# Kernel optimization log

Hardware: AMD Instinct MI355X
Metric: run time of the kernel (lower is better)

## Reference

```python
import jax, jax.numpy as jnp
import numpy as np

D_MODEL = 1024
N_HEADS = 16
DEPTH = D_MODEL // N_HEADS
P_FEAT = 64
NEG_BIG = -1.0e9


def setup_inputs() -> dict:
    key = jax.random.key(0)
    ks = jax.random.split(key, 12)
    B, S = 4, 2048
    s = 1.0 / np.sqrt(D_MODEL)
    return {
        "q": jax.random.normal(ks[0], (B, S, D_MODEL), jnp.float32),
        "k": jax.random.normal(ks[1], (B, S, D_MODEL), jnp.float32),
        "v": jax.random.normal(ks[2], (B, S, D_MODEL), jnp.float32),
        "protocol_features": jax.random.normal(ks[3], (B, P_FEAT), jnp.float32),
        "mask": jax.random.randint(ks[4], (B, 1, 1, S), 0, 2).astype(jnp.float32),
        "wq": jax.random.normal(ks[5], (D_MODEL, D_MODEL), jnp.float32) * s,
        "bq": jnp.zeros((D_MODEL,), jnp.float32),
        "wk": jax.random.normal(ks[6], (D_MODEL, D_MODEL), jnp.float32) * s,
        "bk": jnp.zeros((D_MODEL,), jnp.float32),
        "wv": jax.random.normal(ks[7], (D_MODEL, D_MODEL), jnp.float32) * s,
        "bv": jnp.zeros((D_MODEL,), jnp.float32),
        "wg": jax.random.normal(ks[8], (P_FEAT, N_HEADS), jnp.float32) * (1.0 / np.sqrt(P_FEAT)),
        "bg": jnp.zeros((N_HEADS,), jnp.float32),
    }


def _split_heads(x, B):
    # [B,S,d_model] -> [B,H,S,depth]
    return x.reshape(B, -1, N_HEADS, DEPTH).transpose(0, 2, 1, 3)


def reference(q, k, v, protocol_features, mask, wq, bq, wk, bk, wv, bv, wg, bg):
    B = q.shape[0]
    qh = _split_heads(q @ wq + bq, B)
    kh = _split_heads(k @ wk + bk, B)
    vh = _split_heads(v @ wv + bv, B)
    # scaled QK^T: [B,H,S,S]
    logits = jnp.einsum("bhqd,bhkd->bhqk", qh, kh) / jnp.sqrt(jnp.float32(DEPTH))
    # per-head protocol gate (sigmoid), broadcast over q/k positions
    validity = jax.nn.sigmoid(protocol_features @ wg + bg)  # [B,H]
    logits = logits * validity[:, :, None, None]
    logits = logits + mask * NEG_BIG
    attn = jax.nn.softmax(logits, axis=-1)
    out = jnp.einsum("bhqk,bhkd->bhqd", attn, vh)
    concat = out.transpose(0, 2, 1, 3).reshape(B, -1, D_MODEL)
    return concat, attn
```

## Files before the change

### kernel.cpp

```cpp
#include <hip/hip_runtime.h>

#define S_LEN 2048
#define NB 4
#define NH 16
#define BHN 64
#define DM 1024
#define DEP 64
#define MROWS 8192

typedef __attribute__((ext_vector_type(8))) short short8;
typedef __attribute__((ext_vector_type(4))) short s16x4;
typedef __attribute__((ext_vector_type(4))) float f32x4;

#define MFMA_BF16(a, b, c) __builtin_amdgcn_mfma_f32_16x16x32_bf16((a), (b), (c), 0, 0, 0)

__device__ __forceinline__ void mfma16(const s16x4& a, const s16x4& b, f32x4& c) {
  asm("v_mfma_f32_16x16x16_bf16 %0, %1, %2, %0" : "+v"(c) : "v"(a), "v"(b));
}

typedef __attribute__((address_space(1))) const void* as1cv;
typedef __attribute__((address_space(3))) void* as3v;

__device__ __forceinline__ void gld16(const void* g, void* l) {
  __builtin_amdgcn_global_load_lds((as1cv)g, (as3v)l, 16, 0, 0);
}

__device__ __forceinline__ unsigned short f2bf(float f) {
  unsigned u = __float_as_uint(f);
  u += 0x7fffu + ((u >> 16) & 1u);
  return (unsigned short)(u >> 16);
}

__device__ __forceinline__ unsigned cvtpk(float a, float b) {
  unsigned r;
  asm("v_cvt_pk_bf16_f32 %0, %1, %2" : "=v"(r) : "v"(a), "v"(b));
  return r;
}

__device__ __forceinline__ int SWZ(int row, int gran) {
  return row * 64 + ((gran ^ (row & 7)) << 3);
}

__global__ void gate_kernel(const float* __restrict__ pf, const float* __restrict__ wg,
                            const float* __restrict__ bg, float* __restrict__ validity) {
  int t = threadIdx.x;
  int b = t >> 4, h = t & 15;
  float s = bg[h];
  for (int i = 0; i < 64; i++) s += pf[b * 64 + i] * wg[i * NH + h];
  validity[t] = 1.0f / (1.0f + __expf(-s));
}

__global__ __launch_bounds__(256) void wt_kernel(const float* __restrict__ W,
                                                 unsigned short* __restrict__ Wt) {
  __shared__ unsigned short T[64][72];
  int k0 = blockIdx.x * 64, n0 = blockIdx.y * 64;
  int t = threadIdx.x;
  int r = t >> 2, c4 = (t & 3) * 16;
  for (int j = 0; j < 16; j += 4) {
    float4 v = *(const float4*)&W[(size_t)(k0 + r) * DM + n0 + c4 + j];
    T[r][c4 + j + 0] = f2bf(v.x); T[r][c4 + j + 1] = f2bf(v.y);
    T[r][c4 + j + 2] = f2bf(v.z); T[r][c4 + j + 3] = f2bf(v.w);
  }
  __syncthreads();
  union { unsigned short us[16]; uint4 v[2]; } o;
  for (int j = 0; j < 16; j++) o.us[j] = T[c4 + j][r];
  *(uint4*)&Wt[(size_t)(n0 + r) * DM + k0 + c4] = o.v[0];
  *(uint4*)&Wt[(size_t)(n0 + r) * DM + k0 + c4 + 8] = o.v[1];
}

__global__ __launch_bounds__(256) void vt_kernel(const unsigned short* __restrict__ vh,
                                                 unsigned short* __restrict__ vhT) {
  __shared__ unsigned short T[64][72];
  int bh = blockIdx.y;
  int s0 = blockIdx.x * 64;
  int t = threadIdx.x;
  int r = t >> 2, c4 = (t & 3) * 16;
  const unsigned short* src = vh + ((size_t)bh * S_LEN + s0 + r) * DEP + c4;
  *(uint4*)&T[r][c4] = *(const uint4*)src;
  *(uint4*)&T[r][c4 + 8] = *(const uint4*)(src + 8);
  __syncthreads();
  union { unsigned short us[16]; uint4 v[2]; } o;
  for (int j = 0; j < 16; j++) o.us[j] = T[c4 + j][r];
  unsigned short* dst = vhT + ((size_t)bh * DEP + r) * S_LEN + s0 + c4;
  *(uint4*)dst = o.v[0];
  *(uint4*)(dst + 8) = o.v[1];
}

__global__ __launch_bounds__(256) void proj3_gemm(const float* __restrict__ Xq,
                                                  const float* __restrict__ Xk,
                                                  const float* __restrict__ Xv,
                                                  const unsigned short* __restrict__ BtBase,
                                                  const float* __restrict__ bq,
                                                  const float* __restrict__ bk,
                                                  const float* __restrict__ bv,
                                                  unsigned short* __restrict__ Ybase) {
  __shared__ unsigned short As[128 * 64], Bs[128 * 64];
  const int K = DM;
  int z = blockIdx.z;
  const float* X = (z == 0) ? Xq : (z == 1) ? Xk : Xv;
  const float* bias = (z == 0) ? bq : (z == 1) ? bk : bv;
  const unsigned short* Bt = BtBase + (size_t)z * DM * DM;
  unsigned short* Y = Ybase + (size_t)z * MROWS * DM;

  int tid = threadIdx.x, w = tid >> 6, l = tid & 63, g = l >> 4, lc = l & 15;
  int r0 = blockIdx.x * 128, c0 = blockIdx.y * 128;
  int wr = w >> 1, wc = w & 1;
  int lrow = l >> 3, lcol = (l & 7) * 8;
  int sr = tid >> 3, sc = (tid & 7) * 8;
  f32x4 acc[4][4] = {};
  for (int k0 = 0; k0 < K; k0 += 64) {
    __syncthreads();
    for (int i = 0; i < 4; i++) {
      int row = (w * 4 + i) * 8 + lrow;
      gld16(Bt + (size_t)(c0 + row) * K + k0 + lcol, &Bs[(w * 4 + i) * 512]);
    }
    for (int i = 0; i < 4; i++) {
      int row = i * 32 + sr;
      const float* src = X + (size_t)(r0 + row) * K + k0 + sc;
      float4 a0 = *(const float4*)src;
      float4 a1 = *(const float4*)(src + 4);
      uint4 o = {cvtpk(a0.x, a0.y), cvtpk(a0.z, a0.w),
                 cvtpk(a1.x, a1.y), cvtpk(a1.z, a1.w)};
      *(uint4*)&As[row * 64 + sc] = o;
    }
    __syncthreads();
    for (int kk = 0; kk < 2; kk++) {
      short8 a[4], b[4];
      for (int m = 0; m < 4; m++)
        a[m] = *(const short8*)&As[(wr * 64 + m * 16 + lc) * 64 + kk * 32 + g * 8];
      for (int n = 0; n < 4; n++)
        b[n] = *(const short8*)&Bs[(wc * 64 + n * 16 + lc) * 64 + kk * 32 + g * 8];
      for (int m = 0; m < 4; m++)
        for (int n = 0; n < 4; n++)
          acc[m][n] = MFMA_BF16(a[m], b[n], acc[m][n]);
    }
  }
  for (int n = 0; n < 4; n++) {
    int c = c0 + wc * 64 + n * 16 + lc;
    float bi = bias[c];
    int h = c >> 6, d = c & 63;
    for (int m = 0; m < 4; m++) {
      int rowbase = r0 + wr * 64 + m * 16 + g * 4;
      for (int r = 0; r < 4; r++) {
        int row = rowbase + r;
        int b_ = row >> 11, s = row & 2047;
        Y[(((size_t)b_ * NH + h) * S_LEN + s) * DEP + d] = f2bf(acc[m][n][r] + bi);
      }
    }
  }
}

__global__ __launch_bounds__(512) void attn_fused(const unsigned short* __restrict__ qh,
                                                  const unsigned short* __restrict__ kh,
                                                  const unsigned short* __restrict__ vhT,
                                                  const float* __restrict__ validity,
                                                  const float* __restrict__ mask,
                                                  float* __restrict__ concat,
                                                  float* __restrict__ attn) {
  __shared__ unsigned short Qs[128 * 64];
  __shared__ unsigned short KV[4][64 * 64];
  __shared__ unsigned short MsB[S_LEN];

  int id = blockIdx.x;
  int cxcd = id & 7, j = id >> 3;
  int bh = cxcd * 8 + (j >> 4);
  int q0 = (j & 15) * 128;
  int b = bh >> 4, h = bh & 15;

  int tid = threadIdx.x, w = tid >> 6, l = tid & 63, g = l >> 4, lc = l & 15;
  int srow = l >> 3;
  int sgran = (l & 7) ^ srow;
  float scale = validity[bh] * 0.125f * 1.44269504f;
  for (int i = tid; i < S_LEN; i += 512)
    MsB[i] = f2bf(mask[(size_t)b * S_LEN + i] * (-1.44269504e9f));

  const unsigned short* qb = qh + (size_t)bh * S_LEN * DEP;
  const unsigned short* kb = kh + (size_t)bh * S_LEN * DEP;
  const unsigned short* vb = vhT + (size_t)bh * DEP * S_LEN;
  int qrow = w * 16 + lc;

  unsigned short* B0 = &KV[0][0];
  unsigned short* B1 = &KV[2][0];
  for (int i = 0; i < 2; i++)
    gld16(qb + (size_t)(q0 + i * 64 + w * 8 + srow) * DEP + sgran * 8,
          &Qs[(i * 64 + w * 8) * 64]);
  for (int i = 0; i < 2; i++)
    gld16(kb + (size_t)(i * 64 + w * 8 + srow) * DEP + sgran * 8,
          B0 + (i * 64 + w * 8) * 64);
  __syncthreads();
  short8 aq0 = *(const short8*)&Qs[SWZ(qrow, g)];
  short8 aq1 = *(const short8*)&Qs[SWZ(qrow, 4 + g)];

  float ell = 0.f;
  for (int kt2 = 0; kt2 < 16; kt2++) {
    const int cb = kt2 & 1;
    unsigned short* cur = cb ? B1 : B0;
    if (kt2 < 15) {
      unsigned short* nxt = cb ? B0 : B1;
      for (int i = 0; i < 2; i++)
        gld16(kb + (size_t)((kt2 + 1) * 128 + i * 64 + w * 8 + srow) * DEP + sgran * 8,
              nxt + (i * 64 + w * 8) * 64);
    }
    for (int f = 0; f < 8; f++) {
      int krow = f * 16 + lc;
      short8 ak0 = *(const short8*)&cur[SWZ(krow, g)];
      short8 ak1 = *(const short8*)&cur[SWZ(krow, 4 + g)];
      f32x4 c = {};
      __builtin_amdgcn_s_setprio(1);
      c = MFMA_BF16(ak0, aq0, c);
      c = MFMA_BF16(ak1, aq1, c);
      __builtin_amdgcn_s_setprio(0);
      uint2 mu = *(const uint2*)&MsB[kt2 * 128 + f * 16 + g * 4];
      float mb0 = __uint_as_float(mu.x << 16);
      float mb1 = __uint_as_float(mu.x & 0xFFFF0000u);
      float mb2 = __uint_as_float(mu.y << 16);
      float mb3 = __uint_as_float(mu.y & 0xFFFF0000u);
      ell += exp2f(fmaf(c[0], scale, mb0)) + exp2f(fmaf(c[1], scale, mb1)) +
             exp2f(fmaf(c[2], scale, mb2)) + exp2f(fmaf(c[3], scale, mb3));
    }
    __builtin_amdgcn_sched_barrier(0);
    asm volatile("s_waitcnt vmcnt(0)" ::: "memory");
    __builtin_amdgcn_sched_barrier(0);
    __builtin_amdgcn_s_barrier();
  }
  ell += __shfl_xor(ell, 16, 64);
  ell += __shfl_xor(ell, 32, 64);
  float rinv = 1.0f / ell;

  gld16(kb + (size_t)(w * 8 + srow) * DEP + sgran * 8, &KV[0][w * 512]);
  gld16(vb + (size_t)(w * 8 + srow) * S_LEN + sgran * 8, &KV[2][w * 512]);
  __syncthreads();

  float* arow = attn + ((size_t)bh * S_LEN + q0 + w * 16 + lc) * S_LEN + g * 4;

  f32x4 O[4] = {};
#pragma unroll 2
  for (int kt = 0; kt < 32; kt++) {
    const int cb = kt & 1;
    if (kt < 31) {
      gld16(kb + (size_t)((kt + 1) * 64 + w * 8 + srow) * DEP + sgran * 8,
            &KV[cb ^ 1][w * 512]);
      gld16(vb + (size_t)(w * 8 + srow) * S_LEN + (kt + 1) * 64 + sgran * 8,
            &KV[2 + (cb ^ 1)][w * 512]);
    }
    s16x4 pa[4];
#pragma unroll
    for (int f = 0; f < 4; f++) {
      int krow = f * 16 + lc;
      short8 ak0 = *(const short8*)&KV[cb][SWZ(krow, g)];
      short8 ak1 = *(const short8*)&KV[cb][SWZ(krow, 4 + g)];
      f32x4 c = {};
      __builtin_amdgcn_s_setprio(1);
      c = MFMA_BF16(ak0, aq0, c);
      c = MFMA_BF16(ak1, aq1, c);
      __builtin_amdgcn_s_setprio(0);
      uint2 mu = *(const uint2*)&MsB[kt * 64 + f * 16 + g * 4];
      float mb0 = __uint_as_float(mu.x << 16);
      float mb1 = __uint_as_float(mu.x & 0xFFFF0000u);
      float mb2 = __uint_as_float(mu.y << 16);
      float mb3 = __uint_as_float(mu.y & 0xFFFF0000u);
      float p0 = exp2f(fmaf(c[0], scale, mb0)) * rinv;
      float p1 = exp2f(fmaf(c[1], scale, mb1)) * rinv;
      float p2 = exp2f(fmaf(c[2], scale, mb2)) * rinv;
      float p3 = exp2f(fmaf(c[3], scale, mb3)) * rinv;
      *(f32x4*)(arow + kt * 64 + f * 16) = f32x4{p0, p1, p2, p3};
      union { unsigned u[2]; s16x4 s; } pk;
      pk.u[0] = cvtpk(p0, p1);
      pk.u[1] = cvtpk(p2, p3);
      pa[f] = pk.s;
    }
    __builtin_amdgcn_s_setprio(1);
#pragma unroll
    for (int f = 0; f < 4; f++) {
#pragma unroll
      for (int n = 0; n < 4; n++) {
        int vrow = n * 16 + lc;
        int gran = (f * 2 + (g >> 1)) ^ (vrow & 7);
        s16x4 bv = *(const s16x4*)&KV[2 + cb][vrow * 64 + gran * 8 + (g & 1) * 4];
        mfma16(pa[f], bv, O[n]);
      }
    }
    __builtin_amdgcn_s_setprio(0);
    __builtin_amdgcn_sched_barrier(0);
    if (kt < 31) { asm volatile("s_waitcnt vmcnt(4)" ::: "memory"); }
    __builtin_amdgcn_sched_barrier(0);
    __builtin_amdgcn_s_barrier();
  }
  for (int n = 0; n < 4; n++)
    for (int r = 0; r < 4; r++)
      concat[((size_t)b * S_LEN + q0 + w * 16 + g * 4 + r) * DM + h * DEP + n * 16 + lc] =
          O[n][r];
}

extern "C" void kernel_launch(void* const* d_in, const int* in_sizes, int n_in,
                              void* d_out, int out_size, void* d_ws, size_t ws_size,
                              hipStream_t stream) {
  const float* q    = (const float*)d_in[0];
  const float* k    = (const float*)d_in[1];
  const float* v    = (const float*)d_in[2];
  const float* pf   = (const float*)d_in[3];
  const float* mask = (const float*)d_in[4];
  const float* wq   = (const float*)d_in[5];
  const float* bq   = (const float*)d_in[6];
  const float* wk   = (const float*)d_in[7];
  const float* bk   = (const float*)d_in[8];
  const float* wv   = (const float*)d_in[9];
  const float* bv   = (const float*)d_in[10];
  const float* wg   = (const float*)d_in[11];
  const float* bg   = (const float*)d_in[12];

  float* concat = (float*)d_out;
  float* attn   = concat + (size_t)NB * S_LEN * DM;

  unsigned short* wqT = (unsigned short*)attn;
  unsigned short* wkT = wqT + (size_t)DM * DM;
  unsigned short* wvT = wkT + (size_t)DM * DM;

  float* validity = (float*)d_ws;
  unsigned short* qhp = (unsigned short*)((char*)d_ws + 4096);
  unsigned short* khp = qhp + (size_t)MROWS * DM;
  unsigned short* vhp = khp + (size_t)MROWS * DM;
  unsigned short* vhT = vhp + (size_t)MROWS * DM;

  gate_kernel<<<1, 64, 0, stream>>>(pf, wg, bg, validity);

  wt_kernel<<<dim3(16, 16), 256, 0, stream>>>(wq, wqT);
  wt_kernel<<<dim3(16, 16), 256, 0, stream>>>(wk, wkT);
  wt_kernel<<<dim3(16, 16), 256, 0, stream>>>(wv, wvT);

  proj3_gemm<<<dim3(64, 8, 3), 256, 0, stream>>>(q, k, v, wqT, bq, bk, bv, qhp);

  vt_kernel<<<dim3(32, 64), 256, 0, stream>>>(vhp, vhT);

  attn_fused<<<1024, 512, 0, stream>>>(qhp, khp, vhT, validity, mask, concat, attn);
}
```

Measured before the change: 456.6 us.

## Triple-buffer K/V in attention pass two and remap projection blocks per XCD

The second attention pass now uses a three-stage ring of K/V tiles in a shared LDS pool, so loads are issued two tiles ahead and the wait allows more loads in flight. The Q tile and the first-pass buffers are aliased into the same pool to keep LDS usage the same. Separately, the projection GEMM moves to a 1D grid where each XCD (chip partition) gets a contiguous set of row tiles across all columns, aiming to improve L2 reuse of the activation rows. The vmcnt thresholds must match the per-thread load counts exactly, and dropping the unroll pragma may change scheduling.

```diff
diff --git a/kernel.cpp b/kernel.cpp
--- a/kernel.cpp
+++ b/kernel.cpp
@@ -96,14 +96,20 @@
                                                   unsigned short* __restrict__ Ybase) {
   __shared__ unsigned short As[128 * 64], Bs[128 * 64];
   const int K = DM;
-  int z = blockIdx.z;
+  int id = blockIdx.x;
+  int cx = id & 7;
+  int local = id >> 3;
+  int z = local >> 6;
+  int rem = local & 63;
+  int r0 = (cx * 8 + (rem >> 3)) * 128;
+  int c0 = (rem & 7) * 128;
+
   const float* X = (z == 0) ? Xq : (z == 1) ? Xk : Xv;
   const float* bias = (z == 0) ? bq : (z == 1) ? bk : bv;
   const unsigned short* Bt = BtBase + (size_t)z * DM * DM;
   unsigned short* Y = Ybase + (size_t)z * MROWS * DM;
 
   int tid = threadIdx.x, w = tid >> 6, l = tid & 63, g = l >> 4, lc = l & 15;
-  int r0 = blockIdx.x * 128, c0 = blockIdx.y * 128;
   int wr = w >> 1, wc = w & 1;
   int lrow = l >> 3, lcol = (l & 7) * 8;
   int sr = tid >> 3, sc = (tid & 7) * 8;
@@ -157,8 +163,7 @@
                                                   const float* __restrict__ mask,
                                                   float* __restrict__ concat,
                                                   float* __restrict__ attn) {
-  __shared__ unsigned short Qs[128 * 64];
-  __shared__ unsigned short KV[4][64 * 64];
+  __shared__ unsigned short POOL[6 * 4096];
   __shared__ unsigned short MsB[S_LEN];
 
   int id = blockIdx.x;
@@ -179,17 +184,17 @@
   const unsigned short* vb = vhT + (size_t)bh * DEP * S_LEN;
   int qrow = w * 16 + lc;
 
-  unsigned short* B0 = &KV[0][0];
-  unsigned short* B1 = &KV[2][0];
+  unsigned short* B0 = &POOL[2 * 4096];
+  unsigned short* B1 = &POOL[4 * 4096];
   for (int i = 0; i < 2; i++)
     gld16(qb + (size_t)(q0 + i * 64 + w * 8 + srow) * DEP + sgran * 8,
-          &Qs[(i * 64 + w * 8) * 64]);
+          &POOL[(i * 64 + w * 8) * 64]);
   for (int i = 0; i < 2; i++)
     gld16(kb + (size_t)(i * 64 + w * 8 + srow) * DEP + sgran * 8,
           B0 + (i * 64 + w * 8) * 64);
   __syncthreads();
-  short8 aq0 = *(const short8*)&Qs[SWZ(qrow, g)];
-  short8 aq1 = *(const short8*)&Qs[SWZ(qrow, 4 + g)];
+  short8 aq0 = *(const short8*)&POOL[SWZ(qrow, g)];
+  short8 aq1 = *(const short8*)&POOL[SWZ(qrow, 4 + g)];
 
   float ell = 0.f;
   for (int kt2 = 0; kt2 < 16; kt2++) {
@@ -227,28 +232,31 @@
   ell += __shfl_xor(ell, 32, 64);
   float rinv = 1.0f / ell;
 
-  gld16(kb + (size_t)(w * 8 + srow) * DEP + sgran * 8, &KV[0][w * 512]);
-  gld16(vb + (size_t)(w * 8 + srow) * S_LEN + sgran * 8, &KV[2][w * 512]);
+  gld16(kb + (size_t)(w * 8 + srow) * DEP + sgran * 8, &POOL[0 * 4096 + w * 512]);
+  gld16(vb + (size_t)(w * 8 + srow) * S_LEN + sgran * 8, &POOL[1 * 4096 + w * 512]);
+  gld16(kb + (size_t)(64 + w * 8 + srow) * DEP + sgran * 8, &POOL[2 * 4096 + w * 512]);
+  gld16(vb + (size_t)(w * 8 + srow) * S_LEN + 64 + sgran * 8, &POOL[3 * 4096 + w * 512]);
   __syncthreads();
 
   float* arow = attn + ((size_t)bh * S_LEN + q0 + w * 16 + lc) * S_LEN + g * 4;
 
   f32x4 O[4] = {};
-#pragma unroll 2
   for (int kt = 0; kt < 32; kt++) {
-    const int cb = kt & 1;
-    if (kt < 31) {
-      gld16(kb + (size_t)((kt + 1) * 64 + w * 8 + srow) * DEP + sgran * 8,
-            &KV[cb ^ 1][w * 512]);
-      gld16(vb + (size_t)(w * 8 + srow) * S_LEN + (kt + 1) * 64 + sgran * 8,
-            &KV[2 + (cb ^ 1)][w * 512]);
-    }
+    if (kt < 30) {
+      int pr = ((kt + 2) % 3) * 2;
+      gld16(kb + (size_t)((kt + 2) * 64 + w * 8 + srow) * DEP + sgran * 8,
+            &POOL[pr * 4096 + w * 512]);
+      gld16(vb + (size_t)(w * 8 + srow) * S_LEN + (kt + 2) * 64 + sgran * 8,
+            &POOL[(pr + 1) * 4096 + w * 512]);
+    }
+    const unsigned short* Kp = &POOL[(kt % 3) * 2 * 4096];
+    const unsigned short* Vp = Kp + 4096;
     s16x4 pa[4];
 #pragma unroll
     for (int f = 0; f < 4; f++) {
       int krow = f * 16 + lc;
-      short8 ak0 = *(const short8*)&KV[cb][SWZ(krow, g)];
-      short8 ak1 = *(const short8*)&KV[cb][SWZ(krow, 4 + g)];
+      short8 ak0 = *(const short8*)&Kp[SWZ(krow, g)];
+      short8 ak1 = *(const short8*)&Kp[SWZ(krow, 4 + g)];
       f32x4 c = {};
       __builtin_amdgcn_s_setprio(1);
       c = MFMA_BF16(ak0, aq0, c);
@@ -276,15 +284,22 @@
       for (int n = 0; n < 4; n++) {
         int vrow = n * 16 + lc;
         int gran = (f * 2 + (g >> 1)) ^ (vrow & 7);
-        s16x4 bv = *(const s16x4*)&KV[2 + cb][vrow * 64 + gran * 8 + (g & 1) * 4];
+        s16x4 bv = *(const s16x4*)&Vp[vrow * 64 + gran * 8 + (g & 1) * 4];
         mfma16(pa[f], bv, O[n]);
       }
     }
     __builtin_amdgcn_s_setprio(0);
-    __builtin_amdgcn_sched_barrier(0);
-    if (kt < 31) { asm volatile("s_waitcnt vmcnt(4)" ::: "memory"); }
-    __builtin_amdgcn_sched_barrier(0);
-    __builtin_amdgcn_s_barrier();
+    if (kt < 30) {
+      __builtin_amdgcn_sched_barrier(0);
+      asm volatile("s_waitcnt vmcnt(10)" ::: "memory");
+      __builtin_amdgcn_sched_barrier(0);
+      __builtin_amdgcn_s_barrier();
+    } else if (kt == 30) {
+      __builtin_amdgcn_sched_barrier(0);
+      asm volatile("s_waitcnt vmcnt(8)" ::: "memory");
+      __builtin_amdgcn_sched_barrier(0);
+      __builtin_amdgcn_s_barrier();
+    }
   }
   for (int n = 0; n < 4; n++)
     for (int r = 0; r < 4; r++)
@@ -328,7 +343,7 @@
   wt_kernel<<<dim3(16, 16), 256, 0, stream>>>(wk, wkT);
   wt_kernel<<<dim3(16, 16), 256, 0, stream>>>(wv, wvT);
 
-  proj3_gemm<<<dim3(64, 8, 3), 256, 0, stream>>>(q, k, v, wqT, bq, bk, bv, qhp);
+  proj3_gemm<<<1536, 256, 0, stream>>>(q, k, v, wqT, bq, bk, bv, qhp);
 
   vt_kernel<<<dim3(32, 64), 256, 0, stream>>>(vhp, vhT);
 
```

Result: no change. 461.7 us (+1.1%).

## Compact unmasked key indices and skip masked keys in softmax denominator pass

Applied to the files above, without the earlier changes.

Builds a per-block compacted list of unmasked key positions using a wave ballot, a prefix popcount and an LDS atomic counter, then gathers only those K rows for the first pass that computes the softmax row sum. Masked keys add roughly zero to the sum, so with a random mask about half of the K tiles and exp evaluations are skipped. The trade is a gather-style load, extra setup and barriers, and a loop trip count that depends on the data.

```diff
diff --git a/kernel.cpp b/kernel.cpp
--- a/kernel.cpp
+++ b/kernel.cpp
@@ -7,6 +7,7 @@
 #define DM 1024
 #define DEP 64
 #define MROWS 8192
+#define NEGB (-1.44269504e9f)
 
 typedef __attribute__((ext_vector_type(8))) short short8;
 typedef __attribute__((ext_vector_type(4))) short s16x4;
@@ -160,6 +161,8 @@
   __shared__ unsigned short Qs[128 * 64];
   __shared__ unsigned short KV[4][64 * 64];
   __shared__ unsigned short MsB[S_LEN];
+  __shared__ unsigned short Xs[S_LEN];
+  __shared__ int cnt;
 
   int id = blockIdx.x;
   int cxcd = id & 7, j = id >> 3;
@@ -171,35 +174,57 @@
   int srow = l >> 3;
   int sgran = (l & 7) ^ srow;
   float scale = validity[bh] * 0.125f * 1.44269504f;
-  for (int i = tid; i < S_LEN; i += 512)
-    MsB[i] = f2bf(mask[(size_t)b * S_LEN + i] * (-1.44269504e9f));
 
   const unsigned short* qb = qh + (size_t)bh * S_LEN * DEP;
   const unsigned short* kb = kh + (size_t)bh * S_LEN * DEP;
   const unsigned short* vb = vhT + (size_t)bh * DEP * S_LEN;
   int qrow = w * 16 + lc;
 
-  unsigned short* B0 = &KV[0][0];
-  unsigned short* B1 = &KV[2][0];
+  if (tid == 0) cnt = 0;
   for (int i = 0; i < 2; i++)
     gld16(qb + (size_t)(q0 + i * 64 + w * 8 + srow) * DEP + sgran * 8,
           &Qs[(i * 64 + w * 8) * 64]);
-  for (int i = 0; i < 2; i++)
-    gld16(kb + (size_t)(i * 64 + w * 8 + srow) * DEP + sgran * 8,
-          B0 + (i * 64 + w * 8) * 64);
-  __syncthreads();
+  __syncthreads();
+  const unsigned short negbf = f2bf(NEGB);
+  for (int r = 0; r < 4; r++) {
+    int pos = w * 256 + r * 64 + l;
+    bool keep = (mask[(size_t)b * S_LEN + pos] == 0.0f);
+    MsB[pos] = keep ? (unsigned short)0 : negbf;
+    unsigned long long bal = __ballot(keep);
+    int prefix = __popcll(bal & ((1ull << l) - 1ull));
+    int wcount = __popcll(bal);
+    int base = 0;
+    if (l == 0) base = atomicAdd(&cnt, wcount);
+    base = __shfl(base, 0, 64);
+    if (keep) Xs[base + prefix] = (unsigned short)pos;
+  }
+  __syncthreads();
+  int cntv = cnt;
+  int padded = (cntv + 127) & ~127;
+  int nt1v = padded >> 7;
+  for (int i = cntv + tid; i < padded; i += 512) Xs[i] = (unsigned short)0x8000;
   short8 aq0 = *(const short8*)&Qs[SWZ(qrow, g)];
   short8 aq1 = *(const short8*)&Qs[SWZ(qrow, 4 + g)];
+  __syncthreads();
+
+  unsigned short* B0 = &KV[0][0];
+  unsigned short* B1 = &KV[2][0];
+  for (int i = 0; i < 2; i++) {
+    int rowi = Xs[i * 64 + w * 8 + srow] & 0x7FFF;
+    gld16(kb + (size_t)rowi * DEP + sgran * 8, B0 + (i * 64 + w * 8) * 64);
+  }
+  __syncthreads();
 
   float ell = 0.f;
-  for (int kt2 = 0; kt2 < 16; kt2++) {
+  for (int kt2 = 0; kt2 < nt1v; kt2++) {
     const int cb = kt2 & 1;
     unsigned short* cur = cb ? B1 : B0;
-    if (kt2 < 15) {
+    if (kt2 + 1 < nt1v) {
       unsigned short* nxt = cb ? B0 : B1;
-      for (int i = 0; i < 2; i++)
-        gld16(kb + (size_t)((kt2 + 1) * 128 + i * 64 + w * 8 + srow) * DEP + sgran * 8,
-              nxt + (i * 64 + w * 8) * 64);
+      for (int i = 0; i < 2; i++) {
+        int rowi = Xs[(kt2 + 1) * 128 + i * 64 + w * 8 + srow] & 0x7FFF;
+        gld16(kb + (size_t)rowi * DEP + sgran * 8, nxt + (i * 64 + w * 8) * 64);
+      }
     }
     for (int f = 0; f < 8; f++) {
       int krow = f * 16 + lc;
@@ -210,11 +235,11 @@
       c = MFMA_BF16(ak0, aq0, c);
       c = MFMA_BF16(ak1, aq1, c);
       __builtin_amdgcn_s_setprio(0);
-      uint2 mu = *(const uint2*)&MsB[kt2 * 128 + f * 16 + g * 4];
-      float mb0 = __uint_as_float(mu.x << 16);
-      float mb1 = __uint_as_float(mu.x & 0xFFFF0000u);
-      float mb2 = __uint_as_float(mu.y << 16);
-      float mb3 = __uint_as_float(mu.y & 0xFFFF0000u);
+      s16x4 iv = *(const s16x4*)&Xs[kt2 * 128 + f * 16 + g * 4];
+      float mb0 = (iv[0] < 0) ? NEGB : 0.0f;
+      float mb1 = (iv[1] < 0) ? NEGB : 0.0f;
+      float mb2 = (iv[2] < 0) ? NEGB : 0.0f;
+      float mb3 = (iv[3] < 0) ? NEGB : 0.0f;
       ell += exp2f(fmaf(c[0], scale, mb0)) + exp2f(fmaf(c[1], scale, mb1)) +
              exp2f(fmaf(c[2], scale, mb2)) + exp2f(fmaf(c[3], scale, mb3));
     }
```

Measured after the change: 476.1 us. 1.04x slower.
